# Kernel tuning notes

Measured on AMD Instinct MI355X. Metric: run time of the kernel, lower is better.

Reference implementation:

```python
import jax, jax.numpy as jnp
import numpy as np

N = 50000      # nodes
E = 500000     # edges
D = 32         # hidden_dim
ED = 16        # edge_dim
MSG_IN = 2 * D + ED
EPS = 1e-5


def setup_inputs() -> dict:
    key = jax.random.key(0)
    ks = jax.random.split(key, 16)

    def lin(k, fan_in, fan_out):
        s = 1.0 / np.sqrt(fan_in)
        return jax.random.uniform(k, (fan_in, fan_out), jnp.float32, -s, s)

    return {
        "t": jnp.zeros((), jnp.float32),
        "h": jax.random.normal(ks[0], (N, D), jnp.float32),
        "edge_attr": jax.random.normal(ks[1], (E, ED), jnp.float32),
        "Q": jax.random.normal(ks[2], (E, D, D), jnp.float32) * (1.0 / np.sqrt(D)),
        # msg_net: 2-layer MLP (Linear -> ReLU -> Linear)
        "W1": lin(ks[3], MSG_IN, D), "b1": jnp.zeros((D,), jnp.float32),
        "W2": lin(ks[4], D, D),      "b2": jnp.zeros((D,), jnp.float32),
        # dynamics_net: Linear(2D,D) -> LayerNorm -> SiLU -> Linear(D,D) -> Tanh
        "Wd1": lin(ks[5], 2 * D, D), "bd1": jnp.zeros((D,), jnp.float32),
        "ln_g": jnp.ones((D,), jnp.float32), "ln_b": jnp.zeros((D,), jnp.float32),
        "Wd2": lin(ks[6], D, D),     "bd2": jnp.zeros((D,), jnp.float32),
        "edge_index": jax.random.randint(ks[7], (2, E), 0, N, jnp.int64),
    }


def reference(t, h, edge_attr, Q, W1, b1, W2, b2, Wd1, bd1, ln_g, ln_b, Wd2, bd2, edge_index):
    row, col = edge_index[0], edge_index[1]
    # sheaf transport of source states: Q_uv @ h[col]
    h_transported = jnp.einsum('eij,ej->ei', Q, h[col])          # [E, D]
    msg_input = jnp.concatenate([h[row], h_transported, edge_attr], axis=-1)  # [E, 2D+ED]
    hidden = jax.nn.relu(msg_input @ W1 + b1)
    messages = hidden @ W2 + b2                                   # [E, D]
    agg = jax.ops.segment_sum(messages, row, num_segments=N)      # [N, D]
    x = jnp.concatenate([h, agg], axis=-1) @ Wd1 + bd1            # [N, D]
    mu = jnp.mean(x, axis=-1, keepdims=True)
    var = jnp.mean((x - mu) ** 2, axis=-1, keepdims=True)
    x = (x - mu) * jax.lax.rsqrt(var + EPS) * ln_g + ln_b
    x = jax.nn.silu(x)
    return jnp.tanh(x @ Wd2 + bd2)                                # dh/dt [N, D]
```

## Files before the change

### kernel.cpp

```cpp
#include <hip/hip_runtime.h>
#include <math.h>

#define N_NODES 50000
#define E_EDGES 500000
#define D 32
#define ED 16
#define MSG_LEN 112

__global__ __launch_bounds__(256) void edge_kernel(
    const float* __restrict__ h, const float* __restrict__ edge_attr,
    const float* __restrict__ Q, const float* __restrict__ W1,
    const float* __restrict__ b1, const float* __restrict__ W2,
    const float* __restrict__ b2, const int* __restrict__ eidx,
    float* __restrict__ agg)
{
    const int lane = threadIdx.x & 63;
    const int wib  = threadIdx.x >> 6;
    const int gwave = blockIdx.x * 4 + wib;
    const int nwaves = gridDim.x * 4;

    const int o   = lane & 31;
    const int hh  = lane >> 5;
    const int g   = lane >> 3;
    const int sub = lane & 7;

    float w1c[40];
#pragma unroll
    for (int i = 0; i < 40; ++i) w1c[i] = W1[(hh * 40 + i) * D + o];
    float w2c[16];
#pragma unroll
    for (int i = 0; i < 16; ++i) w2c[i] = W2[(hh * 16 + i) * D + o];
    const float b1o = b1[o];
    const float b2o = b2[o];

    __shared__ float msg_s[4][MSG_LEN];
    float* m = msg_s[wib];

    for (int e = gwave; e < E_EDGES; e += nwaves) {
        const int row = eidx[e];
        const int col = eidx[E_EDGES + e];

        const float4 hc = *reinterpret_cast<const float4*>(h + (size_t)col * D + sub * 4);

        const float* qe = Q + (size_t)e * (D * D);
        float acc[4];
#pragma unroll
        for (int k = 0; k < 4; ++k) {
            const float4 q = *reinterpret_cast<const float4*>(qe + k * 256 + lane * 4);
            acc[k] = q.x * hc.x + q.y * hc.y + q.z * hc.z + q.w * hc.w;
        }
#pragma unroll
        for (int mm = 1; mm <= 4; mm <<= 1) {
#pragma unroll
            for (int k = 0; k < 4; ++k) acc[k] += __shfl_xor(acc[k], mm);
        }

        if (lane < D)               m[lane] = h[(size_t)row * D + lane];
        else if (lane < D + ED)     m[64 + (lane - D)] = edge_attr[(size_t)e * ED + (lane - D)];
        if (sub == 0) {
#pragma unroll
            for (int k = 0; k < 4; ++k) m[D + k * 8 + g] = acc[k];
        }
        asm volatile("s_waitcnt lgkmcnt(0)" ::: "memory");

        float s = 0.f;
        const float4* mv4 = reinterpret_cast<const float4*>(m + hh * 40);
#pragma unroll
        for (int i4 = 0; i4 < 10; ++i4) {
            const float4 mv = mv4[i4];
            s = fmaf(mv.x, w1c[4 * i4 + 0], s);
            s = fmaf(mv.y, w1c[4 * i4 + 1], s);
            s = fmaf(mv.z, w1c[4 * i4 + 2], s);
            s = fmaf(mv.w, w1c[4 * i4 + 3], s);
        }
        s += __shfl_xor(s, 32);
        s = fmaxf(s + b1o, 0.f);

        if (lane < D) m[80 + lane] = s;
        asm volatile("s_waitcnt lgkmcnt(0)" ::: "memory");

        float tv = 0.f;
        const float4* hv4 = reinterpret_cast<const float4*>(m + 80 + hh * 16);
#pragma unroll
        for (int i4 = 0; i4 < 4; ++i4) {
            const float4 hv = hv4[i4];
            tv = fmaf(hv.x, w2c[4 * i4 + 0], tv);
            tv = fmaf(hv.y, w2c[4 * i4 + 1], tv);
            tv = fmaf(hv.z, w2c[4 * i4 + 2], tv);
            tv = fmaf(hv.w, w2c[4 * i4 + 3], tv);
        }
        tv += __shfl_xor(tv, 32);
        tv += b2o;

        if (lane < D) atomicAdd(&agg[(size_t)row * D + lane], tv);
    }
}

__global__ __launch_bounds__(256) void node_kernel(
    const float* __restrict__ h, const float* __restrict__ agg,
    const float* __restrict__ Wd1, const float* __restrict__ bd1,
    const float* __restrict__ ln_g, const float* __restrict__ ln_b,
    const float* __restrict__ Wd2, const float* __restrict__ bd2,
    float* __restrict__ out)
{
    __shared__ float sWd1[64 * 32];
    __shared__ float sWd2[32 * 32];
    __shared__ float xbuf[4][64];

    for (int i = threadIdx.x; i < 64 * 32; i += 256) sWd1[i] = Wd1[i];
    for (int i = threadIdx.x; i < 32 * 32; i += 256) sWd2[i] = Wd2[i];
    __syncthreads();

    const int tid  = blockIdx.x * 256 + threadIdx.x;
    const int n    = tid >> 5;
    const int o    = tid & 31;
    const int wib  = threadIdx.x >> 6;
    const int lane = threadIdx.x & 63;
    if (n >= N_NODES) return;

    const float* hn = h   + (size_t)n * D;
    const float* an = agg + (size_t)n * D;

    float x = bd1[o];
#pragma unroll
    for (int k4 = 0; k4 < 8; ++k4) {
        const float4 hv = *reinterpret_cast<const float4*>(hn + k4 * 4);
        x = fmaf(hv.x, sWd1[(k4 * 4 + 0) * 32 + o], x);
        x = fmaf(hv.y, sWd1[(k4 * 4 + 1) * 32 + o], x);
        x = fmaf(hv.z, sWd1[(k4 * 4 + 2) * 32 + o], x);
        x = fmaf(hv.w, sWd1[(k4 * 4 + 3) * 32 + o], x);
    }
#pragma unroll
    for (int k4 = 0; k4 < 8; ++k4) {
        const float4 av = *reinterpret_cast<const float4*>(an + k4 * 4);
        x = fmaf(av.x, sWd1[(32 + k4 * 4 + 0) * 32 + o], x);
        x = fmaf(av.y, sWd1[(32 + k4 * 4 + 1) * 32 + o], x);
        x = fmaf(av.z, sWd1[(32 + k4 * 4 + 2) * 32 + o], x);
        x = fmaf(av.w, sWd1[(32 + k4 * 4 + 3) * 32 + o], x);
    }

    float mu = x;
#pragma unroll
    for (int mm = 1; mm <= 16; mm <<= 1) mu += __shfl_xor(mu, mm);
    mu *= (1.0f / 32.0f);
    const float dx = x - mu;
    float var = dx * dx;
#pragma unroll
    for (int mm = 1; mm <= 16; mm <<= 1) var += __shfl_xor(var, mm);
    var *= (1.0f / 32.0f);
    float xs = dx * rsqrtf(var + 1e-5f);
    xs = xs * ln_g[o] + ln_b[o];
    xs = xs / (1.0f + __expf(-xs));

    xbuf[wib][lane] = xs;
    asm volatile("s_waitcnt lgkmcnt(0)" ::: "memory");

    float y = bd2[o];
    const float* xb = &xbuf[wib][lane & 32];
#pragma unroll
    for (int k4 = 0; k4 < 8; ++k4) {
        const float4 xv = *reinterpret_cast<const float4*>(xb + k4 * 4);
        y = fmaf(xv.x, sWd2[(k4 * 4 + 0) * 32 + o], y);
        y = fmaf(xv.y, sWd2[(k4 * 4 + 1) * 32 + o], y);
        y = fmaf(xv.z, sWd2[(k4 * 4 + 2) * 32 + o], y);
        y = fmaf(xv.w, sWd2[(k4 * 4 + 3) * 32 + o], y);
    }
    out[(size_t)n * D + o] = tanhf(y);
}

extern "C" void kernel_launch(void* const* d_in, const int* in_sizes, int n_in,
                              void* d_out, int out_size, void* d_ws, size_t ws_size,
                              hipStream_t stream) {
    const float* h         = (const float*)d_in[1];
    const float* edge_attr = (const float*)d_in[2];
    const float* Q         = (const float*)d_in[3];
    const float* W1        = (const float*)d_in[4];
    const float* b1        = (const float*)d_in[5];
    const float* W2        = (const float*)d_in[6];
    const float* b2        = (const float*)d_in[7];
    const float* Wd1       = (const float*)d_in[8];
    const float* bd1       = (const float*)d_in[9];
    const float* ln_g      = (const float*)d_in[10];
    const float* ln_b      = (const float*)d_in[11];
    const float* Wd2       = (const float*)d_in[12];
    const float* bd2       = (const float*)d_in[13];
    const int*   eidx      = (const int*)d_in[14];

    float* agg = (float*)d_ws;
    hipMemsetAsync(agg, 0, (size_t)N_NODES * D * sizeof(float), stream);

    edge_kernel<<<2048, 256, 0, stream>>>(h, edge_attr, Q, W1, b1, W2, b2, eidx, agg);
    node_kernel<<<(N_NODES * D + 255) / 256, 256, 0, stream>>>(
        h, agg, Wd1, bd1, ln_g, ln_b, Wd2, bd2, (float*)d_out);
}
```

Baseline: 491.2 us.

## Process two edges per wave iteration with prefetched indices and vectorized gathers

Each wave now handles a pair of consecutive edges per iteration. The Q loads for both edges are issued up front, and the next pair's row/col indices are prefetched with int2 loads. The h[row] and edge_attr gathers become float4 loads spread across lane groups, and the explicit s_waitcnt fences are removed on the assumption that the compiler orders LDS accesses within a wave. This aims to raise memory-level parallelism on the Q stream and interleave the two independent FMA chains. The cost is higher register pressure and reliance on implicit wave-level LDS ordering.

After: 500.4 us. Within noise of the previous version (+1.9%).

```diff
diff --git a/kernel.cpp b/kernel.cpp
--- a/kernel.cpp
+++ b/kernel.cpp
@@ -33,66 +33,128 @@
     const float b1o = b1[o];
     const float b2o = b2[o];
 
-    __shared__ float msg_s[4][MSG_LEN];
-    float* m = msg_s[wib];
-
-    for (int e = gwave; e < E_EDGES; e += nwaves) {
-        const int row = eidx[e];
-        const int col = eidx[E_EDGES + e];
-
-        const float4 hc = *reinterpret_cast<const float4*>(h + (size_t)col * D + sub * 4);
-
-        const float* qe = Q + (size_t)e * (D * D);
-        float acc[4];
+    __shared__ __align__(16) float msg_s[4][2][MSG_LEN];
+    float* m0 = msg_s[wib][0];
+    float* m1 = msg_s[wib][1];
+
+    const long long step = 2LL * nwaves;
+    long long e0 = 2LL * gwave;
+
+    int2 rowp = *reinterpret_cast<const int2*>(eidx + e0);
+    int2 colp = *reinterpret_cast<const int2*>(eidx + E_EDGES + e0);
+
+    for (; e0 < E_EDGES; e0 += step) {
+        const long long e1 = e0 + 1;
+        const int row0 = rowp.x, row1 = rowp.y;
+        const int col0 = colp.x, col1 = colp.y;
+
+        const float4 hc0 = *reinterpret_cast<const float4*>(h + (size_t)col0 * D + sub * 4);
+        const float4 hc1 = *reinterpret_cast<const float4*>(h + (size_t)col1 * D + sub * 4);
+
+        if (lane < 8) {
+            const float4 hv = *reinterpret_cast<const float4*>(h + (size_t)row0 * D + lane * 4);
+            *reinterpret_cast<float4*>(m0 + lane * 4) = hv;
+        } else if (lane < 16) {
+            const int l = lane - 8;
+            const float4 hv = *reinterpret_cast<const float4*>(h + (size_t)row1 * D + l * 4);
+            *reinterpret_cast<float4*>(m1 + l * 4) = hv;
+        } else if (lane < 20) {
+            const int l = lane - 16;
+            const float4 ev = *reinterpret_cast<const float4*>(edge_attr + (size_t)e0 * ED + l * 4);
+            *reinterpret_cast<float4*>(m0 + 64 + l * 4) = ev;
+        } else if (lane < 24) {
+            const int l = lane - 20;
+            const float4 ev = *reinterpret_cast<const float4*>(edge_attr + (size_t)e1 * ED + l * 4);
+            *reinterpret_cast<float4*>(m1 + 64 + l * 4) = ev;
+        }
+
+        const float* qe0 = Q + (size_t)e0 * (D * D);
+        const float* qe1 = Q + (size_t)e1 * (D * D);
+        float4 qa[4], qb[4];
+#pragma unroll
+        for (int k = 0; k < 4; ++k)
+            qa[k] = *reinterpret_cast<const float4*>(qe0 + k * 256 + lane * 4);
+#pragma unroll
+        for (int k = 0; k < 4; ++k)
+            qb[k] = *reinterpret_cast<const float4*>(qe1 + k * 256 + lane * 4);
+
+        const long long en = e0 + step;
+        if (en < E_EDGES) {
+            rowp = *reinterpret_cast<const int2*>(eidx + en);
+            colp = *reinterpret_cast<const int2*>(eidx + E_EDGES + en);
+        }
+
+        float acc0[4], acc1[4];
 #pragma unroll
         for (int k = 0; k < 4; ++k) {
-            const float4 q = *reinterpret_cast<const float4*>(qe + k * 256 + lane * 4);
-            acc[k] = q.x * hc.x + q.y * hc.y + q.z * hc.z + q.w * hc.w;
+            acc0[k] = qa[k].x * hc0.x + qa[k].y * hc0.y + qa[k].z * hc0.z + qa[k].w * hc0.w;
+            acc1[k] = qb[k].x * hc1.x + qb[k].y * hc1.y + qb[k].z * hc1.z + qb[k].w * hc1.w;
         }
 #pragma unroll
         for (int mm = 1; mm <= 4; mm <<= 1) {
 #pragma unroll
-            for (int k = 0; k < 4; ++k) acc[k] += __shfl_xor(acc[k], mm);
-        }
-
-        if (lane < D)               m[lane] = h[(size_t)row * D + lane];
-        else if (lane < D + ED)     m[64 + (lane - D)] = edge_attr[(size_t)e * ED + (lane - D)];
+            for (int k = 0; k < 4; ++k) {
+                acc0[k] += __shfl_xor(acc0[k], mm);
+                acc1[k] += __shfl_xor(acc1[k], mm);
+            }
+        }
         if (sub == 0) {
 #pragma unroll
-            for (int k = 0; k < 4; ++k) m[D + k * 8 + g] = acc[k];
-        }
-        asm volatile("s_waitcnt lgkmcnt(0)" ::: "memory");
-
-        float s = 0.f;
-        const float4* mv4 = reinterpret_cast<const float4*>(m + hh * 40);
+            for (int k = 0; k < 4; ++k) {
+                m0[D + k * 8 + g] = acc0[k];
+                m1[D + k * 8 + g] = acc1[k];
+            }
+        }
+
+        float s0 = 0.f, s1 = 0.f;
+        const float4* ma4 = reinterpret_cast<const float4*>(m0 + hh * 40);
+        const float4* mb4 = reinterpret_cast<const float4*>(m1 + hh * 40);
 #pragma unroll
         for (int i4 = 0; i4 < 10; ++i4) {
-            const float4 mv = mv4[i4];
-            s = fmaf(mv.x, w1c[4 * i4 + 0], s);
-            s = fmaf(mv.y, w1c[4 * i4 + 1], s);
-            s = fmaf(mv.z, w1c[4 * i4 + 2], s);
-            s = fmaf(mv.w, w1c[4 * i4 + 3], s);
-        }
-        s += __shfl_xor(s, 32);
-        s = fmaxf(s + b1o, 0.f);
-
-        if (lane < D) m[80 + lane] = s;
-        asm volatile("s_waitcnt lgkmcnt(0)" ::: "memory");
-
-        float tv = 0.f;
-        const float4* hv4 = reinterpret_cast<const float4*>(m + 80 + hh * 16);
+            const float4 va = ma4[i4];
+            const float4 vb = mb4[i4];
+            s0 = fmaf(va.x, w1c[4 * i4 + 0], s0);
+            s1 = fmaf(vb.x, w1c[4 * i4 + 0], s1);
+            s0 = fmaf(va.y, w1c[4 * i4 + 1], s0);
+            s1 = fmaf(vb.y, w1c[4 * i4 + 1], s1);
+            s0 = fmaf(va.z, w1c[4 * i4 + 2], s0);
+            s1 = fmaf(vb.z, w1c[4 * i4 + 2], s1);
+            s0 = fmaf(va.w, w1c[4 * i4 + 3], s0);
+            s1 = fmaf(vb.w, w1c[4 * i4 + 3], s1);
+        }
+        s0 += __shfl_xor(s0, 32);
+        s1 += __shfl_xor(s1, 32);
+        s0 = fmaxf(s0 + b1o, 0.f);
+        s1 = fmaxf(s1 + b1o, 0.f);
+
+        if (lane < 32) m0[80 + o] = s0;
+        else           m1[80 + o] = s1;
+
+        float t0 = 0.f, t1 = 0.f;
+        const float4* ha4 = reinterpret_cast<const float4*>(m0 + 80 + hh * 16);
+        const float4* hb4 = reinterpret_cast<const float4*>(m1 + 80 + hh * 16);
 #pragma unroll
         for (int i4 = 0; i4 < 4; ++i4) {
-            const float4 hv = hv4[i4];
-            tv = fmaf(hv.x, w2c[4 * i4 + 0], tv);
-            tv = fmaf(hv.y, w2c[4 * i4 + 1], tv);
-            tv = fmaf(hv.z, w2c[4 * i4 + 2], tv);
-            tv = fmaf(hv.w, w2c[4 * i4 + 3], tv);
-        }
-        tv += __shfl_xor(tv, 32);
-        tv += b2o;
-
-        if (lane < D) atomicAdd(&agg[(size_t)row * D + lane], tv);
+            const float4 va = ha4[i4];
+            const float4 vb = hb4[i4];
+            t0 = fmaf(va.x, w2c[4 * i4 + 0], t0);
+            t1 = fmaf(vb.x, w2c[4 * i4 + 0], t1);
+            t0 = fmaf(va.y, w2c[4 * i4 + 1], t0);
+            t1 = fmaf(vb.y, w2c[4 * i4 + 1], t1);
+            t0 = fmaf(va.z, w2c[4 * i4 + 2], t0);
+            t1 = fmaf(vb.z, w2c[4 * i4 + 2], t1);
+            t0 = fmaf(va.w, w2c[4 * i4 + 3], t0);
+            t1 = fmaf(vb.w, w2c[4 * i4 + 3], t1);
+        }
+        t0 += __shfl_xor(t0, 32);
+        t1 += __shfl_xor(t1, 32);
+        t0 += b2o;
+        t1 += b2o;
+
+        if (lane < 32) {
+            atomicAdd(&agg[(size_t)row0 * D + o], t0);
+            atomicAdd(&agg[(size_t)row1 * D + o], t1);
+        }
     }
 }
 
@@ -153,7 +215,6 @@
     xs = xs / (1.0f + __expf(-xs));
 
     xbuf[wib][lane] = xs;
-    asm volatile("s_waitcnt lgkmcnt(0)" ::: "memory");
 
     float y = bd2[o];
     const float* xb = &xbuf[wib][lane & 32];
```

## Double-buffer edge loads in registers and stream Q with nontemporal loads

Applied to the files above, without the earlier changes.

Restructures the edge loop into a two-stage software pipeline: the Q, h[col], h[row] and edge_attr loads for the next edge are issued into a second register stage while the current edge is computed. Q is read with nontemporal loads, and the transported vector is written to shared memory as a single float4 by permuting the W1 rows to match. The explicit s_waitcnt fences between LDS writes and reads are removed, so correctness relies on wave-synchronous LDS ordering. The extra register stage raises register pressure and may reduce occupancy.

Measured after the change: 446.7 us. 9.1% less time.

```diff
diff --git a/kernel.cpp b/kernel.cpp
--- a/kernel.cpp
+++ b/kernel.cpp
@@ -5,7 +5,23 @@
 #define E_EDGES 500000
 #define D 32
 #define ED 16
-#define MSG_LEN 112
+#define NBLK 2048
+#define NW_TOTAL (NBLK * 4)
+
+typedef float vf4 __attribute__((ext_vector_type(4)));
+
+struct Stage {
+    vf4 q0, q1, q2, q3;
+    vf4 hc;
+    vf4 st;
+};
+
+__device__ __forceinline__ int2 ld_idx(const int* __restrict__ eidx, long long e) {
+    int2 rc;
+    rc.x = eidx[e];
+    rc.y = eidx[E_EDGES + e];
+    return rc;
+}
 
 __global__ __launch_bounds__(256) void edge_kernel(
     const float* __restrict__ h, const float* __restrict__ edge_attr,
@@ -17,7 +33,6 @@
     const int lane = threadIdx.x & 63;
     const int wib  = threadIdx.x >> 6;
     const int gwave = blockIdx.x * 4 + wib;
-    const int nwaves = gridDim.x * 4;
 
     const int o   = lane & 31;
     const int hh  = lane >> 5;
@@ -26,73 +41,121 @@
 
     float w1c[40];
 #pragma unroll
-    for (int i = 0; i < 40; ++i) w1c[i] = W1[(hh * 40 + i) * D + o];
+    for (int i = 0; i < 40; ++i) {
+        const int p = hh * 40 + i;
+        int f;
+        if (p < 32)      f = p;
+        else if (p < 64) f = 32 + ((p - 32) & 3) * 8 + ((p - 32) >> 2);
+        else             f = p;
+        w1c[i] = W1[f * D + o];
+    }
     float w2c[16];
 #pragma unroll
     for (int i = 0; i < 16; ++i) w2c[i] = W2[(hh * 16 + i) * D + o];
     const float b1o = b1[o];
     const float b2o = b2[o];
 
-    __shared__ float msg_s[4][MSG_LEN];
+    __shared__ __align__(16) float msg_s[4][112];
     float* m = msg_s[wib];
 
-    for (int e = gwave; e < E_EDGES; e += nwaves) {
-        const int row = eidx[e];
-        const int col = eidx[E_EDGES + e];
-
-        const float4 hc = *reinterpret_cast<const float4*>(h + (size_t)col * D + sub * 4);
-
-        const float* qe = Q + (size_t)e * (D * D);
-        float acc[4];
-#pragma unroll
-        for (int k = 0; k < 4; ++k) {
-            const float4 q = *reinterpret_cast<const float4*>(qe + k * 256 + lane * 4);
-            acc[k] = q.x * hc.x + q.y * hc.y + q.z * hc.z + q.w * hc.w;
-        }
+    const long long nw = NW_TOTAL;
+    long long e = gwave;
+    int2 rcc = ld_idx(eidx, e);
+
+    auto issue = [&](Stage& S, long long ee, int row, int col)
+        __attribute__((always_inline)) {
+        const float* qe = Q + (size_t)ee * (D * D);
+        S.hc = *(const vf4*)(h + (size_t)col * D + sub * 4);
+        if (lane < 12) {
+            const float* gsrc = (lane < 8)
+                ? (h + (size_t)row * D + lane * 4)
+                : (edge_attr + (size_t)ee * ED + (lane - 8) * 4);
+            S.st = *(const vf4*)gsrc;
+        }
+        S.q0 = __builtin_nontemporal_load((const vf4*)(qe + 0 * 256 + lane * 4));
+        S.q1 = __builtin_nontemporal_load((const vf4*)(qe + 1 * 256 + lane * 4));
+        S.q2 = __builtin_nontemporal_load((const vf4*)(qe + 2 * 256 + lane * 4));
+        S.q3 = __builtin_nontemporal_load((const vf4*)(qe + 3 * 256 + lane * 4));
+    };
+
+    auto compute = [&](const Stage& S, int row)
+        __attribute__((always_inline)) {
+        if (lane < 12) {
+            float* dst = (lane < 8) ? (m + lane * 4) : (m + 64 + (lane - 8) * 4);
+            *(vf4*)dst = S.st;
+        }
+        float a0 = S.q0.x * S.hc.x + S.q0.y * S.hc.y + S.q0.z * S.hc.z + S.q0.w * S.hc.w;
+        float a1 = S.q1.x * S.hc.x + S.q1.y * S.hc.y + S.q1.z * S.hc.z + S.q1.w * S.hc.w;
+        float a2 = S.q2.x * S.hc.x + S.q2.y * S.hc.y + S.q2.z * S.hc.z + S.q2.w * S.hc.w;
+        float a3 = S.q3.x * S.hc.x + S.q3.y * S.hc.y + S.q3.z * S.hc.z + S.q3.w * S.hc.w;
 #pragma unroll
         for (int mm = 1; mm <= 4; mm <<= 1) {
-#pragma unroll
-            for (int k = 0; k < 4; ++k) acc[k] += __shfl_xor(acc[k], mm);
-        }
-
-        if (lane < D)               m[lane] = h[(size_t)row * D + lane];
-        else if (lane < D + ED)     m[64 + (lane - D)] = edge_attr[(size_t)e * ED + (lane - D)];
+            a0 += __shfl_xor(a0, mm);
+            a1 += __shfl_xor(a1, mm);
+            a2 += __shfl_xor(a2, mm);
+            a3 += __shfl_xor(a3, mm);
+        }
         if (sub == 0) {
-#pragma unroll
-            for (int k = 0; k < 4; ++k) m[D + k * 8 + g] = acc[k];
-        }
-        asm volatile("s_waitcnt lgkmcnt(0)" ::: "memory");
-
+            vf4 t; t.x = a0; t.y = a1; t.z = a2; t.w = a3;
+            *(vf4*)(m + 32 + g * 4) = t;
+        }
         float s = 0.f;
-        const float4* mv4 = reinterpret_cast<const float4*>(m + hh * 40);
+        const vf4* mv = (const vf4*)(m + hh * 40);
 #pragma unroll
         for (int i4 = 0; i4 < 10; ++i4) {
-            const float4 mv = mv4[i4];
-            s = fmaf(mv.x, w1c[4 * i4 + 0], s);
-            s = fmaf(mv.y, w1c[4 * i4 + 1], s);
-            s = fmaf(mv.z, w1c[4 * i4 + 2], s);
-            s = fmaf(mv.w, w1c[4 * i4 + 3], s);
+            const vf4 v = mv[i4];
+            s = fmaf(v.x, w1c[4 * i4 + 0], s);
+            s = fmaf(v.y, w1c[4 * i4 + 1], s);
+            s = fmaf(v.z, w1c[4 * i4 + 2], s);
+            s = fmaf(v.w, w1c[4 * i4 + 3], s);
         }
         s += __shfl_xor(s, 32);
         s = fmaxf(s + b1o, 0.f);
-
-        if (lane < D) m[80 + lane] = s;
-        asm volatile("s_waitcnt lgkmcnt(0)" ::: "memory");
-
-        float tv = 0.f;
-        const float4* hv4 = reinterpret_cast<const float4*>(m + 80 + hh * 16);
+        if (lane < 32) m[80 + o] = s;
+        float t = 0.f;
+        const vf4* hv = (const vf4*)(m + 80 + hh * 16);
 #pragma unroll
         for (int i4 = 0; i4 < 4; ++i4) {
-            const float4 hv = hv4[i4];
-            tv = fmaf(hv.x, w2c[4 * i4 + 0], tv);
-            tv = fmaf(hv.y, w2c[4 * i4 + 1], tv);
-            tv = fmaf(hv.z, w2c[4 * i4 + 2], tv);
-            tv = fmaf(hv.w, w2c[4 * i4 + 3], tv);
-        }
-        tv += __shfl_xor(tv, 32);
-        tv += b2o;
-
-        if (lane < D) atomicAdd(&agg[(size_t)row * D + lane], tv);
+            const vf4 v = hv[i4];
+            t = fmaf(v.x, w2c[4 * i4 + 0], t);
+            t = fmaf(v.y, w2c[4 * i4 + 1], t);
+            t = fmaf(v.z, w2c[4 * i4 + 2], t);
+            t = fmaf(v.w, w2c[4 * i4 + 3], t);
+        }
+        t += __shfl_xor(t, 32);
+        t += b2o;
+        if (lane < 32) atomicAdd(&agg[(size_t)row * D + o], t);
+    };
+
+    const long long e1 = e + nw;
+    int2 rcn = make_int2(0, 0);
+    if (e1 < E_EDGES) rcn = ld_idx(eidx, e1);
+
+    Stage A, B;
+    issue(A, e, rcc.x, rcc.y);
+    if (e1 < E_EDGES) issue(B, e1, rcn.x, rcn.y);
+
+    while (true) {
+        {
+            const long long e2 = e + 2 * nw;
+            int2 rc2 = make_int2(0, 0);
+            if (e2 < E_EDGES) rc2 = ld_idx(eidx, e2);
+            compute(A, rcc.x);
+            if (e2 < E_EDGES) issue(A, e2, rc2.x, rc2.y);
+            rcc = rcn; rcn = rc2;
+            e += nw;
+            if (e >= E_EDGES) break;
+        }
+        {
+            const long long e2 = e + 2 * nw;
+            int2 rc2 = make_int2(0, 0);
+            if (e2 < E_EDGES) rc2 = ld_idx(eidx, e2);
+            compute(B, rcc.x);
+            if (e2 < E_EDGES) issue(B, e2, rc2.x, rc2.y);
+            rcc = rcn; rcn = rc2;
+            e += nw;
+            if (e >= E_EDGES) break;
+        }
     }
 }
 
@@ -153,7 +216,6 @@
     xs = xs / (1.0f + __expf(-xs));
 
     xbuf[wib][lane] = xs;
-    asm volatile("s_waitcnt lgkmcnt(0)" ::: "memory");
 
     float y = bd2[o];
     const float* xb = &xbuf[wib][lane & 32];
@@ -189,7 +251,7 @@
     float* agg = (float*)d_ws;
     hipMemsetAsync(agg, 0, (size_t)N_NODES * D * sizeof(float), stream);
 
-    edge_kernel<<<2048, 256, 0, stream>>>(h, edge_attr, Q, W1, b1, W2, b2, eidx, agg);
+    edge_kernel<<<NBLK, 256, 0, stream>>>(h, edge_attr, Q, W1, b1, W2, b2, eidx, agg);
     node_kernel<<<(N_NODES * D + 255) / 256, 256, 0, stream>>>(
         h, agg, Wd1, bd1, ln_g, ln_b, Wd2, bd2, (float*)d_out);
 }
```
